# Kernel tuning notes

Measured on AMD Instinct MI355X. Metric: run time of the kernel, lower is better.

Reference implementation:

```python
import jax, jax.numpy as jnp
import numpy as np

B, C_IN, N_NODES = 128, 64, 1024
N_TRIPLES = 3 * (N_NODES - 1)  # node 0 is the shared zero vector


def _btc(x, idx, w, b):
    # x: [B, C, N]; idx: [B, 3M]; w: [O, C, 3]; b: [O]
    Bv, C, _ = x.shape
    T = idx.shape[1]
    g = jnp.take_along_axis(x, jnp.broadcast_to(idx[:, None, :], (Bv, C, T)), axis=2)
    g = g.reshape(Bv, C, T // 3, 3)  # stride-3 kernel-3 conv == per-triple contraction
    out = jnp.einsum('bcnk,ock->bon', g, w) + b[None, :, None]
    zero = jnp.zeros((Bv, out.shape[1], 1), dtype=out.dtype)
    return jnp.concatenate([zero, out], axis=2)  # re-prepend zero node -> [B, O, N]


def _tln(x):
    mean = jnp.mean(x, axis=(1, 2), keepdims=True)
    std = jnp.std(x, axis=(1, 2), ddof=1, keepdims=True)  # torch.std is unbiased
    return (x - mean) / (std + 1e-5)


def _tower(x, idx, p):
    x = jax.nn.leaky_relu(_tln(_btc(x, idx, p['w_conv1'], p['b_conv1'])), 0.01)
    x = jax.nn.leaky_relu(_tln(_btc(x, idx, p['w_conv2'], p['b_conv2'])), 0.01)
    x = _tln(_btc(x, idx, p['w_conv3'], p['b_conv3']))
    x = jnp.max(x, axis=2)  # DynamicPooling -> [B, 64]
    x = jax.nn.leaky_relu(x @ p['w_fc1'].T + p['b_fc1'], 0.01)
    return x @ p['w_fc2'].T + p['b_fc2']  # [B, 1]  (Dropout is identity at eval)


def setup_inputs() -> dict:
    key = jax.random.key(0)
    ks = jax.random.split(key, 12)
    s = 0.05
    return {
        'data1': jax.random.normal(ks[0], (B, C_IN, N_NODES), jnp.float32),
        'idx1': jax.random.randint(ks[1], (B, N_TRIPLES, 1), 0, N_NODES, dtype=jnp.int64)
                if jax.config.jax_enable_x64 else
                jax.random.randint(ks[1], (B, N_TRIPLES, 1), 0, N_NODES).astype(jnp.int32),
        'data2': jax.random.normal(ks[2], (B, C_IN, N_NODES), jnp.float32),
        'idx2': jax.random.randint(ks[3], (B, N_TRIPLES, 1), 0, N_NODES).astype(jnp.int32),
        'w_conv1': jax.random.normal(ks[4], (256, C_IN, 3), jnp.float32) * s,
        'b_conv1': jnp.zeros((256,), jnp.float32),
        'w_conv2': jax.random.normal(ks[5], (128, 256, 3), jnp.float32) * s,
        'b_conv2': jnp.zeros((128,), jnp.float32),
        'w_conv3': jax.random.normal(ks[6], (64, 128, 3), jnp.float32) * s,
        'b_conv3': jnp.zeros((64,), jnp.float32),
        'w_fc1': jax.random.normal(ks[7], (32, 64), jnp.float32) * s,
        'b_fc1': jnp.zeros((32,), jnp.float32),
        'w_fc2': jax.random.normal(ks[8], (1, 32), jnp.float32) * s,
        'b_fc2': jnp.zeros((1,), jnp.float32),
    }


def reference(data1, idx1, data2, idx2,
              w_conv1, b_conv1, w_conv2, b_conv2, w_conv3, b_conv3,
              w_fc1, b_fc1, w_fc2, b_fc2):
    p = dict(w_conv1=w_conv1, b_conv1=b_conv1, w_conv2=w_conv2, b_conv2=b_conv2,
             w_conv3=w_conv3, b_conv3=b_conv3, w_fc1=w_fc1, b_fc1=b_fc1,
             w_fc2=w_fc2, b_fc2=b_fc2)
    y1 = _tower(data1, idx1[..., 0], p)
    y2 = _tower(data2, idx2[..., 0], p)
    return jnp.squeeze(jax.nn.sigmoid(y1 - y2), axis=1)  # [B]
```

## Files before the change

### kernel.cpp

```cpp
#include <hip/hip_runtime.h>
#include <math.h>

typedef __attribute__((ext_vector_type(4))) float f32x4;
typedef __attribute__((ext_vector_type(2))) float f32x2;

#define LRELU(x) ((x) > 0.0f ? (x) : 0.01f * (x))

struct __align__(4) Int3 { int x, y, z; };

__device__ __forceinline__ float2 stats_from(const float* sums, int b, float count) {
    float s = sums[2 * b], q = sums[2 * b + 1];
    float mean = s / count;
    float var = (q - s * s / count) / (count - 1.0f);
    var = fmaxf(var, 0.0f);
    return make_float2(mean, 1.0f / (sqrtf(var) + 1e-5f));
}
__device__ __forceinline__ void atomicMaxF(float* a, float v) {
    if (v >= 0.0f) atomicMax((int*)a, __float_as_int(v));
    else           atomicMin((unsigned int*)a, __float_as_uint(v));
}
__device__ __forceinline__ unsigned int fp8x4_nact(unsigned int u, float a, float c) {
    f32x2 lo = __builtin_amdgcn_cvt_pk_f32_fp8(u, false);
    f32x2 hi = __builtin_amdgcn_cvt_pk_f32_fp8(u, true);
    lo = lo * a + c; hi = hi * a + c;
// ... 150 lines not shown
    for (int i = 0; i < 4; i++)
#pragma unroll
        for (int t = 0; t < 4; t++) acc[i][t] = (f32x4){0.f, 0.f, 0.f, 0.f};

    const unsigned char* xb = xT8 + (((size_t)b) << 10) * 64;
    const int* idxb = (b >= 128 ? idxB : idxA) + (size_t)(b & 127) * 3069;

    const int gr = tid >> 1, gh = tid & 1;
    int s0, s1, s2;
    {
        int n = nt0 + gr;
        int t0 = (n == 0) ? 0 : (n - 1);
        const Int3 sv = *(const Int3*)&idxb[3 * t0];
        s0 = sv.x; s1 = sv.y; s2 = sv.z;
    }
    const unsigned char* wrow = wq8 + (size_t)(o0 + gr) * 192;
    const int swz = gr & 7;

    uint4 g0A, g1A, g2A, g3A, w0A, w1A, w2A, w3A;
    uint4 g0B, g1B, g2B, g3B, w0B, w1B, w2B, w3B;

    {
        const int srcA = gh ? s1 : s0;
        const uint4* gp = (const uint4*)(xb + (size_t)srcA * 64);
        g0A = gp[0]; g1A = gp[1]; g2A = gp[2]; g3A = gp[3];
        const uint4* wp = (const uint4*)(wrow + (gh << 6));
        w0A = wp[0]; w1A = wp[1]; w2A = wp[2]; w3A = wp[3];
    }
    if (gh == 0) {
        const uint4* gp = (const uint4*)(xb + (size_t)s2 * 64);
        g0B = gp[0]; g1B = gp[1]; g2B = gp[2]; g3B = gp[3];
        const uint4* wp = (const uint4*)(wrow + 128);
        w0B = wp[0]; w1B = wp[1]; w2B = wp[2]; w3B = wp[3];
    }

    *(uint4*)&gt8[gr * 128 + (((gh << 2) | 0) ^ swz) * 16] = g0A;
    *(uint4*)&gt8[gr * 128 + (((gh << 2) | 1) ^ swz) * 16] = g1A;
    *(uint4*)&gt8[gr * 128 + (((gh << 2) | 2) ^ swz) * 16] = g2A;
    *(uint4*)&gt8[gr * 128 + (((gh << 2) | 3) ^ swz) * 16] = g3A;
    *(uint4*)&wt8[gr * 128 + (((gh << 2) | 0) ^ swz) * 16] = w0A;
    *(uint4*)&wt8[gr * 128 + (((gh << 2) | 1) ^ swz) * 16] = w1A;
    *(uint4*)&wt8[gr * 128 + (((gh << 2) | 2) ^ swz) * 16] = w2A;
    *(uint4*)&wt8[gr * 128 + (((gh << 2) | 3) ^ swz) * 16] = w3A;

#define MFMA_PP(PP) {                                                            \
        ulonglong2 a0v, a1v, a2v, a3v, b0v, b1v, b2v, b3v;                       \
        {                                                                        \
            const int cx = ((((PP) * 4 + quad) ^ blkid) << 4);                   \
            a0v = *(const ulonglong2*)&wt8[(wo * 64 +  0 + l15) * 128 + cx];     \
            a1v = *(const ulonglong2*)&wt8[(wo * 64 + 16 + l15) * 128 + cx];     \
            a2v = *(const ulonglong2*)&wt8[(wo * 64 + 32 + l15) * 128 + cx];     \
            a3v = *(const ulonglong2*)&wt8[(wo * 64 + 48 + l15) * 128 + cx];     \
            b0v = *(const ulonglong2*)&gt8[(wn * 64 +  0 + l15) * 128 + cx];     \
            b1v = *(const ulonglong2*)&gt8[(wn * 64 + 16 + l15) * 128 + cx];     \
            b2v = *(const ulonglong2*)&gt8[(wn * 64 + 32 + l15) * 128 + cx];     \
            b3v = *(const ulonglong2*)&gt8[(wn * 64 + 48 + l15) * 128 + cx];     \
        }                                                                        \
        acc[0][0] = __builtin_amdgcn_mfma_f32_16x16x32_fp8_fp8((long)a0v.x, (long)b0v.x, acc[0][0], 0, 0, 0); \
        acc[0][1] = __builtin_amdgcn_mfma_f32_16x16x32_fp8_fp8((long)a0v.x, (long)b1v.x, acc[0][1], 0, 0, 0); \
        acc[0][2] = __builtin_amdgcn_mfma_f32_16x16x32_fp8_fp8((long)a0v.x, (long)b2v.x, acc[0][2], 0, 0, 0); \
        acc[0][3] = __builtin_amdgcn_mfma_f32_16x16x32_fp8_fp8((long)a0v.x, (long)b3v.x, acc[0][3], 0, 0, 0); \
        acc[1][0] = __builtin_amdgcn_mfma_f32_16x16x32_fp8_fp8((long)a1v.x, (long)b0v.x, acc[1][0], 0, 0, 0); \
        acc[1][1] = __builtin_amdgcn_mfma_f32_16x16x32_fp8_fp8((long)a1v.x, (long)b1v.x, acc[1][1], 0, 0, 0); \
        acc[1][2] = __builtin_amdgcn_mfma_f32_16x16x32_fp8_fp8((long)a1v.x, (long)b2v.x, acc[1][2], 0, 0, 0); \
        acc[1][3] = __builtin_amdgcn_mfma_f32_16x16x32_fp8_fp8((long)a1v.x, (long)b3v.x, acc[1][3], 0, 0, 0); \
        acc[2][0] = __builtin_amdgcn_mfma_f32_16x16x32_fp8_fp8((long)a2v.x, (long)b0v.x, acc[2][0], 0, 0, 0); \
        acc[2][1] = __builtin_amdgcn_mfma_f32_16x16x32_fp8_fp8((long)a2v.x, (long)b1v.x, acc[2][1], 0, 0, 0); \
        acc[2][2] = __builtin_amdgcn_mfma_f32_16x16x32_fp8_fp8((long)a2v.x, (long)b2v.x, acc[2][2], 0, 0, 0); \
        acc[2][3] = __builtin_amdgcn_mfma_f32_16x16x32_fp8_fp8((long)a2v.x, (long)b3v.x, acc[2][3], 0, 0, 0); \
        acc[3][0] = __builtin_amdgcn_mfma_f32_16x16x32_fp8_fp8((long)a3v.x, (long)b0v.x, acc[3][0], 0, 0, 0); \
        acc[3][1] = __builtin_amdgcn_mfma_f32_16x16x32_fp8_fp8((long)a3v.x, (long)b1v.x, acc[3][1], 0, 0, 0); \
        acc[3][2] = __builtin_amdgcn_mfma_f32_16x16x32_fp8_fp8((long)a3v.x, (long)b2v.x, acc[3][2], 0, 0, 0); \
        acc[3][3] = __builtin_amdgcn_mfma_f32_16x16x32_fp8_fp8((long)a3v.x, (long)b3v.x, acc[3][3], 0, 0, 0); \
        acc[0][0] = __builtin_amdgcn_mfma_f32_16x16x32_fp8_fp8((long)a0v.y, (long)b0v.y, acc[0][0], 0, 0, 0); \
        acc[0][1] = __builtin_amdgcn_mfma_f32_16x16x32_fp8_fp8((long)a0v.y, (long)b1v.y, acc[0][1], 0, 0, 0); \
        acc[0][2] = __builtin_amdgcn_mfma_f32_16x16x32_fp8_fp8((long)a0v.y, (long)b2v.y, acc[0][2], 0, 0, 0); \
        acc[0][3] = __builtin_amdgcn_mfma_f32_16x16x32_fp8_fp8((long)a0v.y, (long)b3v.y, acc[0][3], 0, 0, 0); \
        acc[1][0] = __builtin_amdgcn_mfma_f32_16x16x32_fp8_fp8((long)a1v.y, (long)b0v.y, acc[1][0], 0, 0, 0); \
        acc[1][1] = __builtin_amdgcn_mfma_f32_16x16x32_fp8_fp8((long)a1v.y, (long)b1v.y, acc[1][1], 0, 0, 0); \
        acc[1][2] = __builtin_amdgcn_mfma_f32_16x16x32_fp8_fp8((long)a1v.y, (long)b2v.y, acc[1][2], 0, 0, 0); \
        acc[1][3] = __builtin_amdgcn_mfma_f32_16x16x32_fp8_fp8((long)a1v.y, (long)b3v.y, acc[1][3], 0, 0, 0); \
        acc[2][0] = __builtin_amdgcn_mfma_f32_16x16x32_fp8_fp8((long)a2v.y, (long)b0v.y, acc[2][0], 0, 0, 0); \
        acc[2][1] = __builtin_amdgcn_mfma_f32_16x16x32_fp8_fp8((long)a2v.y, (long)b1v.y, acc[2][1], 0, 0, 0); \
        acc[2][2] = __builtin_amdgcn_mfma_f32_16x16x32_fp8_fp8((long)a2v.y, (long)b2v.y, acc[2][2], 0, 0, 0); \
        acc[2][3] = __builtin_amdgcn_mfma_f32_16x16x32_fp8_fp8((long)a2v.y, (long)b3v.y, acc[2][3], 0, 0, 0); \
        acc[3][0] = __builtin_amdgcn_mfma_f32_16x16x32_fp8_fp8((long)a3v.y, (long)b0v.y, acc[3][0], 0, 0, 0); \
        acc[3][1] = __builtin_amdgcn_mfma_f32_16x16x32_fp8_fp8((long)a3v.y, (long)b1v.y, acc[3][1], 0, 0, 0); \
        acc[3][2] = __builtin_amdgcn_mfma_f32_16x16x32_fp8_fp8((long)a3v.y, (long)b2v.y, acc[3][2], 0, 0, 0); \
        acc[3][3] = __builtin_amdgcn_mfma_f32_16x16x32_fp8_fp8((long)a3v.y, (long)b3v.y, acc[3][3], 0, 0, 0); \
    }

    __syncthreads();
    MFMA_PP(0);
    MFMA_PP(1);
    __syncthreads();
    if (gh == 0) {
        *(uint4*)&gt8[gr * 128 + ((0 ^ swz) * 16)] = g0B;
        *(uint4*)&gt8[gr * 128 + ((1 ^ swz) * 16)] = g1B;
        *(uint4*)&gt8[gr * 128 + ((2 ^ swz) * 16)] = g2B;
        *(uint4*)&gt8[gr * 128 + ((3 ^ swz) * 16)] = g3B;
        *(uint4*)&wt8[gr * 128 + ((0 ^ swz) * 16)] = w0B;
        *(uint4*)&wt8[gr * 128 + ((1 ^ swz) * 16)] = w1B;
        *(uint4*)&wt8[gr * 128 + ((2 ^ swz) * 16)] = w2B;
        *(uint4*)&wt8[gr * 128 + ((3 ^ swz) * 16)] = w3B;
    }
    __syncthreads();
    MFMA_PP(0);
#undef MFMA_PP

    __syncthreads();
    unsigned char* eb = gt8;
    float lsum = 0.f, lsq = 0.f;
#pragma unroll
    for (int i = 0; i < 4; i++) {
        const int obl = wo * 64 + i * 16 + quad * 4;
        const int op  = perm128(obl);
        const float4 bv = *(const float4*)(bias + o0 + obl);
#pragma unroll
        for (int t = 0; t < 4; t++) {
            const int nl = wn * 64 + t * 16 + l15;
            float v0 = acc[i][t][0] + bv.x;
            float v1 = acc[i][t][1] + bv.y;
            float v2 = acc[i][t][2] + bv.z;
            float v3 = acc[i][t][3] + bv.w;
            if (nt0 + nl == 0) { v0 = v1 = v2 = v3 = 0.f; }
            lsum += v0 + v1 + v2 + v3;
            lsq  += v0 * v0 + v1 * v1 + v2 * v2 + v3 * v3;
            int r = __builtin_amdgcn_cvt_pk_fp8_f32(v0, v1, 0, false);
            r = __builtin_amdgcn_cvt_pk_fp8_f32(v2, v3, r, true);
            *(unsigned int*)&eb[nl * 128 + (op ^ ((nl & 7) << 4))] = (unsigned int)r;
        }
    }
#pragma unroll
    for (int off = 32; off > 0; off >>= 1) {
        lsum += __shfl_down(lsum, off);
        lsq  += __shfl_down(lsq, off);
    }
    float* red = (float*)wt8;
    if (lane == 0) { red[wave] = lsum; red[4 + wave] = lsq; }
    __syncthreads();
#pragma unroll
    for (int c = 0; c < 4; ++c) {
        const int ch = c * 256 + tid;
        const int row = ch >> 3, off = (ch & 7) << 4;
        uint4 v = *(const uint4*)&eb[row * 128 + (off ^ ((row & 7) << 4))];
        *(uint4*)&out[((size_t)b * 1024 + nt0 + row) * 256 + o0 + off] = v;
    }
    if (tid == 0) {
        atomicAdd(&sums[2 * b + 0], red[0] + red[1] + red[2] + red[3]);
        atomicAdd(&sums[2 * b + 1], red[4] + red[5] + red[6] + red[7]);
    }
}

__global__ __launch_bounds__(256, 3) void conv2_fp8(
    const unsigned char* __restrict__ a1,
    const int* __restrict__ idxA,
    const int* __restrict__ idxB,
    const unsigned char* __restrict__ wq8,
    const float* __restrict__ bias,
    unsigned char* __restrict__ out,
    float* __restrict__ sums)
{
    const int b   = blockIdx.x;
    const int nt0 = blockIdx.z << 7;
    const int tid = threadIdx.x;
    const int lane = tid & 63, wave = tid >> 6;
    const int wo = wave & 1, wn = wave >> 1;
    const int quad = lane >> 4, l15 = lane & 15;
    const int blkid = lane & 7;

    __shared__ __align__(16) unsigned char wt8[128 * 128];
    __shared__ __align__(16) unsigned char gt8[128 * 128];

    f32x4 acc[4][4];
#pragma unroll
    for (int i = 0; i < 4; i++)
#pragma unroll
        for (int t = 0; t < 4; t++) acc[i][t] = (f32x4){0.f, 0.f, 0.f, 0.f};

    const unsigned char* xb = a1 + (((size_t)b) << 10) * 256;
    const int* idxb = (b >= 128 ? idxB : idxA) + (size_t)(b & 127) * 3069;

    const int gr = tid >> 1, gh = tid & 1;
    int si0, si1, si2;
    {
        int n = nt0 + gr;
        int t0 = (n == 0) ? 0 : (n - 1);
        const Int3 sv = *(const Int3*)&idxb[3 * t0];
        si0 = sv.x; si1 = sv.y; si2 = sv.z;
    }
    const unsigned char* wrow = wq8 + (size_t)gr * 768 + gh * 64;
    const int swz = gr & 7;

    uint4 g0A, g1A, g2A, g3A;
    uint4 g0B, g1B, g2B, g3B;

#define LOADC2(S, KC) {                                                          \
        const int j_  = (KC) >> 1;                                               \
        const int c0_ = ((KC) & 1) << 7;                                         \
        const int src_ = (j_ == 0) ? si0 : ((j_ == 1) ? si1 : si2);              \
        const uint4* gp_ = (const uint4*)(xb + (size_t)src_ * 256 + c0_ + gh * 64); \
        g0##S = gp_[0]; g1##S = gp_[1]; g2##S = gp_[2]; g3##S = gp_[3];          \
    }

#define STAGE2(S, KC) {                                                          \
        const uint4* wp_ = (const uint4*)(wrow + (KC) * 128);                    \
        uint4 wv0 = wp_[0], wv1 = wp_[1], wv2 = wp_[2], wv3 = wp_[3];            \
        *(uint4*)&gt8[gr * 128 + (((gh << 2) | 0) ^ swz) * 16] = g0##S;          \
        *(uint4*)&gt8[gr * 128 + (((gh << 2) | 1) ^ swz) * 16] = g1##S;          \
        *(uint4*)&gt8[gr * 128 + (((gh << 2) | 2) ^ swz) * 16] = g2##S;          \
        *(uint4*)&gt8[gr * 128 + (((gh << 2) | 3) ^ swz) * 16] = g3##S;          \
        *(uint4*)&wt8[gr * 128 + (((gh << 2) | 0) ^ swz) * 16] = wv0;            \
        *(uint4*)&wt8[gr * 128 + (((gh << 2) | 1) ^ swz) * 16] = wv1;            \
        *(uint4*)&wt8[gr * 128 + (((gh << 2) | 2) ^ swz) * 16] = wv2;            \
        *(uint4*)&wt8[gr * 128 + (((gh << 2) | 3) ^ swz) * 16] = wv3;            \
    }

#define MFMA_STEP2 {                                                             \
        _Pragma("unroll")                                                        \
        for (int pp = 0; pp < 2; ++pp) {                                         \
            ulonglong2 a0v, a1v, a2v, a3v, b0v, b1v, b2v, b3v;                   \
            {                                                                    \
                const int cx = (((pp * 4 + quad) ^ blkid) << 4);                 \
                a0v = *(const ulonglong2*)&wt8[(wo * 64 +  0 + l15) * 128 + cx]; \
                a1v = *(const ulonglong2*)&wt8[(wo * 64 + 16 + l15) * 128 + cx]; \
                a2v = *(const ulonglong2*)&wt8[(wo * 64 + 32 + l15) * 128 + cx]; \
                a3v = *(const ulonglong2*)&wt8[(wo * 64 + 48 + l15) * 128 + cx]; \
                b0v = *(const ulonglong2*)&gt8[(wn * 64 +  0 + l15) * 128 + cx]; \
                b1v = *(const ulonglong2*)&gt8[(wn * 64 + 16 + l15) * 128 + cx]; \
                b2v = *(const ulonglong2*)&gt8[(wn * 64 + 32 + l15) * 128 + cx]; \
                b3v = *(const ulonglong2*)&gt8[(wn * 64 + 48 + l15) * 128 + cx]; \
            }                                                                    \
            acc[0][0] = __builtin_amdgcn_mfma_f32_16x16x32_fp8_fp8((long)a0v.x, (long)b0v.x, acc[0][0], 0, 0, 0); \
            acc[0][1] = __builtin_amdgcn_mfma_f32_16x16x32_fp8_fp8((long)a0v.x, (long)b1v.x, acc[0][1], 0, 0, 0); \
            acc[0][2] = __builtin_amdgcn_mfma_f32_16x16x32_fp8_fp8((long)a0v.x, (long)b2v.x, acc[0][2], 0, 0, 0); \
            acc[0][3] = __builtin_amdgcn_mfma_f32_16x16x32_fp8_fp8((long)a0v.x, (long)b3v.x, acc[0][3], 0, 0, 0); \
            acc[1][0] = __builtin_amdgcn_mfma_f32_16x16x32_fp8_fp8((long)a1v.x, (long)b0v.x, acc[1][0], 0, 0, 0); \
            acc[1][1] = __builtin_amdgcn_mfma_f32_16x16x32_fp8_fp8((long)a1v.x, (long)b1v.x, acc[1][1], 0, 0, 0); \
            acc[1][2] = __builtin_amdgcn_mfma_f32_16x16x32_fp8_fp8((long)a1v.x, (long)b2v.x, acc[1][2], 0, 0, 0); \
            acc[1][3] = __builtin_amdgcn_mfma_f32_16x16x32_fp8_fp8((long)a1v.x, (long)b3v.x, acc[1][3], 0, 0, 0); \
            acc[2][0] = __builtin_amdgcn_mfma_f32_16x16x32_fp8_fp8((long)a2v.x, (long)b0v.x, acc[2][0], 0, 0, 0); \
            acc[2][1] = __builtin_amdgcn_mfma_f32_16x16x32_fp8_fp8((long)a2v.x, (long)b1v.x, acc[2][1], 0, 0, 0); \
            acc[2][2] = __builtin_amdgcn_mfma_f32_16x16x32_fp8_fp8((long)a2v.x, (long)b2v.x, acc[2][2], 0, 0, 0); \
            acc[2][3] = __builtin_amdgcn_mfma_f32_16x16x32_fp8_fp8((long)a2v.x, (long)b3v.x, acc[2][3], 0, 0, 0); \
            acc[3][0] = __builtin_amdgcn_mfma_f32_16x16x32_fp8_fp8((long)a3v.x, (long)b0v.x, acc[3][0], 0, 0, 0); \
            acc[3][1] = __builtin_amdgcn_mfma_f32_16x16x32_fp8_fp8((long)a3v.x, (long)b1v.x, acc[3][1], 0, 0, 0); \
            acc[3][2] = __builtin_amdgcn_mfma_f32_16x16x32_fp8_fp8((long)a3v.x, (long)b2v.x, acc[3][2], 0, 0, 0); \
            acc[3][3] = __builtin_amdgcn_mfma_f32_16x16x32_fp8_fp8((long)a3v.x, (long)b3v.x, acc[3][3], 0, 0, 0); \
            acc[0][0] = __builtin_amdgcn_mfma_f32_16x16x32_fp8_fp8((long)a0v.y, (long)b0v.y, acc[0][0], 0, 0, 0); \
            acc[0][1] = __builtin_amdgcn_mfma_f32_16x16x32_fp8_fp8((long)a0v.y, (long)b1v.y, acc[0][1], 0, 0, 0); \
            acc[0][2] = __builtin_amdgcn_mfma_f32_16x16x32_fp8_fp8((long)a0v.y, (long)b2v.y, acc[0][2], 0, 0, 0); \
            acc[0][3] = __builtin_amdgcn_mfma_f32_16x16x32_fp8_fp8((long)a0v.y, (long)b3v.y, acc[0][3], 0, 0, 0); \
            acc[1][0] = __builtin_amdgcn_mfma_f32_16x16x32_fp8_fp8((long)a1v.y, (long)b0v.y, acc[1][0], 0, 0, 0); \
            acc[1][1] = __builtin_amdgcn_mfma_f32_16x16x32_fp8_fp8((long)a1v.y, (long)b1v.y, acc[1][1], 0, 0, 0); \
            acc[1][2] = __builtin_amdgcn_mfma_f32_16x16x32_fp8_fp8((long)a1v.y, (long)b2v.y, acc[1][2], 0, 0, 0); \
            acc[1][3] = __builtin_amdgcn_mfma_f32_16x16x32_fp8_fp8((long)a1v.y, (long)b3v.y, acc[1][3], 0, 0, 0); \
            acc[2][0] = __builtin_amdgcn_mfma_f32_16x16x32_fp8_fp8((long)a2v.y, (long)b0v.y, acc[2][0], 0, 0, 0); \
            acc[2][1] = __builtin_amdgcn_mfma_f32_16x16x32_fp8_fp8((long)a2v.y, (long)b1v.y, acc[2][1], 0, 0, 0); \
            acc[2][2] = __builtin_amdgcn_mfma_f32_16x16x32_fp8_fp8((long)a2v.y, (long)b2v.y, acc[2][2], 0, 0, 0); \
            acc[2][3] = __builtin_amdgcn_mfma_f32_16x16x32_fp8_fp8((long)a2v.y, (long)b3v.y, acc[2][3], 0, 0, 0); \
            acc[3][0] = __builtin_amdgcn_mfma_f32_16x16x32_fp8_fp8((long)a3v.y, (long)b0v.y, acc[3][0], 0, 0, 0); \
            acc[3][1] = __builtin_amdgcn_mfma_f32_16x16x32_fp8_fp8((long)a3v.y, (long)b1v.y, acc[3][1], 0, 0, 0); \
            acc[3][2] = __builtin_amdgcn_mfma_f32_16x16x32_fp8_fp8((long)a3v.y, (long)b2v.y, acc[3][2], 0, 0, 0); \
            acc[3][3] = __builtin_amdgcn_mfma_f32_16x16x32_fp8_fp8((long)a3v.y, (long)b3v.y, acc[3][3], 0, 0, 0); \
        }                                                                        \
    }

    LOADC2(A, 0);
    LOADC2(B, 1);
    int kc = 0;
    for (; kc + 2 <= 6; kc += 2) {
        if (kc) __syncthreads();
        STAGE2(A, kc);
        if (kc + 2 < 6) LOADC2(A, kc + 2);
        __syncthreads();
        MFMA_STEP2;
        __syncthreads();
        STAGE2(B, kc + 1);
        if (kc + 3 < 6) LOADC2(B, kc + 3);
        __syncthreads();
        MFMA_STEP2;
    }
#undef LOADC2
#undef STAGE2
#undef MFMA_STEP2

    __syncthreads();
    unsigned char* eb = gt8;
    float lsum = 0.f, lsq = 0.f;
#pragma unroll
    for (int i = 0; i < 4; i++) {
        const int obl = wo * 64 + i * 16 + quad * 4;
        const int op  = perm128(obl);
        const float4 bv = *(const float4*)(bias + obl);
#pragma unroll
        for (int t = 0; t < 4; t++) {
            const int nl = wn * 64 + t * 16 + l15;
            float v0 = acc[i][t][0] + bv.x;
            float v1 = acc[i][t][1] + bv.y;
            float v2 = acc[i][t][2] + bv.z;
            float v3 = acc[i][t][3] + bv.w;
            if (nt0 + nl == 0) { v0 = v1 = v2 = v3 = 0.f; }
            lsum += v0 + v1 + v2 + v3;
            lsq  += v0 * v0 + v1 * v1 + v2 * v2 + v3 * v3;
            int r = __builtin_amdgcn_cvt_pk_fp8_f32(v0, v1, 0, false);
            r = __builtin_amdgcn_cvt_pk_fp8_f32(v2, v3, r, true);
            *(unsigned int*)&eb[nl * 128 + (op ^ ((nl & 7) << 4))] = (unsigned int)r;
        }
    }
#pragma unroll
    for (int off = 32; off > 0; off >>= 1) {
        lsum += __shfl_down(lsum, off);
        lsq  += __shfl_down(lsq, off);
    }
    float* red = (float*)wt8;
    if (lane == 0) { red[wave] = lsum; red[4 + wave] = lsq; }
    __syncthreads();
#pragma unroll
    for (int c = 0; c < 4; ++c) {
        const int ch = c * 256 + tid;
        const int row = ch >> 3, off = (ch & 7) << 4;
        uint4 v = *(const uint4*)&eb[row * 128 + (off ^ ((row & 7) << 4))];
        *(uint4*)&out[((size_t)b * 1024 + nt0 + row) * 128 + off] = v;
    }
    if (tid == 0) {
        atomicAdd(&sums[2 * b + 0], red[0] + red[1] + red[2] + red[3]);
        atomicAdd(&sums[2 * b + 1], red[4] + red[5] + red[6] + red[7]);
    }
}

__global__ __launch_bounds__(256, 3) void conv3_fp8(
    const unsigned char* __restrict__ a2,
    const int* __restrict__ idxA,
    const int* __restrict__ idxB,
    const unsigned char* __restrict__ wq8,
    const float* __restrict__ bias,
    float* __restrict__ sums,
    float* __restrict__ pmax)
{
    const int b   = blockIdx.x;
    const int nt0 = blockIdx.z << 7;
    const int tid = threadIdx.x;
    const int lane = tid & 63, wave = tid >> 6;
    const int wo = wave & 1, wn = wave >> 1;
    const int quad = lane >> 4, l15 = lane & 15;
    const int blkid = lane & 7;

    __shared__ __align__(16) unsigned char wt8[64 * 128];
    __shared__ __align__(16) unsigned char gt8[128 * 128];

    f32x4 acc[2][4];
#pragma unroll
    for (int i = 0; i < 2; i++)
#pragma unroll
        for (int t = 0; t < 4; t++) acc[i][t] = (f32x4){0.f, 0.f, 0.f, 0.f};

    const unsigned char* xb = a2 + (((size_t)b) << 10) * 128;
    const int* idxb = (b >= 128 ? idxB : idxA) + (size_t)(b & 127) * 3069;

    const int gr = tid >> 1, gh = tid & 1;
    int si0, si1, si2;
    {
        int n = nt0 + gr;
        int t0 = (n == 0) ? 0 : (n - 1);
        const Int3 sv = *(const Int3*)&idxb[3 * t0];
        si0 = sv.x; si1 = sv.y; si2 = sv.z;
    }
    const int wr = tid >> 2, wseg = tid & 3;
    const unsigned char* wrow = wq8 + (size_t)wr * 384 + wseg * 32;
    const int gswz = gr & 7, wswz = wr & 7;

    uint4 g0A, g1A, g2A, g3A;
    uint4 g0B, g1B, g2B, g3B;

#define LOADC3(S, KC) {                                                          \
        const int src_ = ((KC) == 0) ? si0 : (((KC) == 1) ? si1 : si2);          \
        const uint4* gp_ = (const uint4*)(xb + (size_t)src_ * 128 + gh * 64);    \
        g0##S = gp_[0]; g1##S = gp_[1]; g2##S = gp_[2]; g3##S = gp_[3];          \
    }

#define STAGE3(S, KC) {                                                          \
        const uint4* wp_ = (const uint4*)(wrow + (KC) * 128);                    \
        uint4 wv0 = wp_[0], wv1 = wp_[1];                                        \
        *(uint4*)&gt8[gr * 128 + (((gh << 2) | 0) ^ gswz) * 16] = g0##S;         \
        *(uint4*)&gt8[gr * 128 + (((gh << 2) | 1) ^ gswz) * 16] = g1##S;         \
        *(uint4*)&gt8[gr * 128 + (((gh << 2) | 2) ^ gswz) * 16] = g2##S;         \
        *(uint4*)&gt8[gr * 128 + (((gh << 2) | 3) ^ gswz) * 16] = g3##S;         \
        *(uint4*)&wt8[wr * 128 + (((wseg << 1) | 0) ^ wswz) * 16] = wv0;         \
        *(uint4*)&wt8[wr * 128 + (((wseg << 1) | 1) ^ wswz) * 16] = wv1;         \
    }

#define MFMA_STEP3 {                                                             \
        _Pragma("unroll")                                                        \
        for (int pp = 0; pp < 2; ++pp) {                                         \
            ulonglong2 a0v, a1v, b0v, b1v, b2v, b3v;                             \
            {                                                                    \
                const int cx = (((pp * 4 + quad) ^ blkid) << 4);                 \
                a0v = *(const ulonglong2*)&wt8[(wo * 32 +  0 + l15) * 128 + cx]; \
                a1v = *(const ulonglong2*)&wt8[(wo * 32 + 16 + l15) * 128 + cx]; \
                b0v = *(const ulonglong2*)&gt8[(wn * 64 +  0 + l15) * 128 + cx]; \
                b1v = *(const ulonglong2*)&gt8[(wn * 64 + 16 + l15) * 128 + cx]; \
                b2v = *(const ulonglong2*)&gt8[(wn * 64 + 32 + l15) * 128 + cx]; \
                b3v = *(const ulonglong2*)&gt8[(wn * 64 + 48 + l15) * 128 + cx]; \
            }                                                                    \
            acc[0][0] = __builtin_amdgcn_mfma_f32_16x16x32_fp8_fp8((long)a0v.x, (long)b0v.x, acc[0][0], 0, 0, 0); \
            acc[0][1] = __builtin_amdgcn_mfma_f32_16x16x32_fp8_fp8((long)a0v.x, (long)b1v.x, acc[0][1], 0, 0, 0); \
            acc[0][2] = __builtin_amdgcn_mfma_f32_16x16x32_fp8_fp8((long)a0v.x, (long)b2v.x, acc[0][2], 0, 0, 0); \
            acc[0][3] = __builtin_amdgcn_mfma_f32_16x16x32_fp8_fp8((long)a0v.x, (long)b3v.x, acc[0][3], 0, 0, 0); \
            acc[1][0] = __builtin_amdgcn_mfma_f32_16x16x32_fp8_fp8((long)a1v.x, (long)b0v.x, acc[1][0], 0, 0, 0); \
            acc[1][1] = __builtin_amdgcn_mfma_f32_16x16x32_fp8_fp8((long)a1v.x, (long)b1v.x, acc[1][1], 0, 0, 0); \
            acc[1][2] = __builtin_amdgcn_mfma_f32_16x16x32_fp8_fp8((long)a1v.x, (long)b2v.x, acc[1][2], 0, 0, 0); \
            acc[1][3] = __builtin_amdgcn_mfma_f32_16x16x32_fp8_fp8((long)a1v.x, (long)b3v.x, acc[1][3], 0, 0, 0); \
            acc[0][0] = __builtin_amdgcn_mfma_f32_16x16x32_fp8_fp8((long)a0v.y, (long)b0v.y, acc[0][0], 0, 0, 0); \
            acc[0][1] = __builtin_amdgcn_mfma_f32_16x16x32_fp8_fp8((long)a0v.y, (long)b1v.y, acc[0][1], 0, 0, 0); \
            acc[0][2] = __builtin_amdgcn_mfma_f32_16x16x32_fp8_fp8((long)a0v.y, (long)b2v.y, acc[0][2], 0, 0, 0); \
            acc[0][3] = __builtin_amdgcn_mfma_f32_16x16x32_fp8_fp8((long)a0v.y, (long)b3v.y, acc[0][3], 0, 0, 0); \
            acc[1][0] = __builtin_amdgcn_mfma_f32_16x16x32_fp8_fp8((long)a1v.y, (long)b0v.y, acc[1][0], 0, 0, 0); \
            acc[1][1] = __builtin_amdgcn_mfma_f32_16x16x32_fp8_fp8((long)a1v.y, (long)b1v.y, acc[1][1], 0, 0, 0); \
            acc[1][2] = __builtin_amdgcn_mfma_f32_16x16x32_fp8_fp8((long)a1v.y, (long)b2v.y, acc[1][2], 0, 0, 0); \
            acc[1][3] = __builtin_amdgcn_mfma_f32_16x16x32_fp8_fp8((long)a1v.y, (long)b3v.y, acc[1][3], 0, 0, 0); \
        }                                                                        \
    }

    LOADC3(A, 0);
    LOADC3(B, 1);
    int kc = 0;
    for (; kc + 2 <= 3; kc += 2) {
        if (kc) __syncthreads();
        STAGE3(A, kc);
        if (kc + 2 < 3) LOADC3(A, kc + 2);
        __syncthreads();
        MFMA_STEP3;
        __syncthreads();
        STAGE3(B, kc + 1);
        __syncthreads();
        MFMA_STEP3;
    }
    {
        __syncthreads();
        STAGE3(A, 2);
        __syncthreads();
        MFMA_STEP3;
    }
#undef LOADC3
#undef STAGE3
#undef MFMA_STEP3

    __syncthreads();
    float lsum = 0.f, lsq = 0.f;
#pragma unroll
    for (int i = 0; i < 2; i++) {
        const int ob = wo * 32 + i * 16 + quad * 4;
        const float4 bv = *(const float4*)(bias + ob);
        float mx0 = -1e30f, mx1 = -1e30f, mx2 = -1e30f, mx3 = -1e30f;
#pragma unroll
        for (int t = 0; t < 4; t++) {
            const int n = nt0 + wn * 64 + t * 16 + l15;
            float v0 = acc[i][t][0] + bv.x;
            float v1 = acc[i][t][1] + bv.y;
            float v2 = acc[i][t][2] + bv.z;
            float v3 = acc[i][t][3] + bv.w;
            if (n == 0) { v0 = v1 = v2 = v3 = 0.f; }
            lsum += v0 + v1 + v2 + v3;
            lsq  += v0 * v0 + v1 * v1 + v2 * v2 + v3 * v3;
            mx0 = fmaxf(mx0, v0); mx1 = fmaxf(mx1, v1);
            mx2 = fmaxf(mx2, v2); mx3 = fmaxf(mx3, v3);
        }
#pragma unroll
        for (int off = 1; off < 16; off <<= 1) {
            mx0 = fmaxf(mx0, __shfl_xor(mx0, off));
            mx1 = fmaxf(mx1, __shfl_xor(mx1, off));
            mx2 = fmaxf(mx2, __shfl_xor(mx2, off));
            mx3 = fmaxf(mx3, __shfl_xor(mx3, off));
        }
        if (l15 == 0) {
            atomicMaxF(&pmax[(size_t)b * 64 + ob + 0], mx0);
            atomicMaxF(&pmax[(size_t)b * 64 + ob + 1], mx1);
            atomicMaxF(&pmax[(size_t)b * 64 + ob + 2], mx2);
            atomicMaxF(&pmax[(size_t)b * 64 + ob + 3], mx3);
        }
    }
#pragma unroll
    for (int off = 32; off > 0; off >>= 1) {
        lsum += __shfl_down(lsum, off);
        lsq  += __shfl_down(lsq, off);
    }
    float* red = (float*)wt8;
    if (lane == 0) { red[wave] = lsum; red[4 + wave] = lsq; }
    __syncthreads();
    if (tid == 0) {
        atomicAdd(&sums[2 * b + 0], red[0] + red[1] + red[2] + red[3]);
        atomicAdd(&sums[2 * b + 1], red[4] + red[5] + red[6] + red[7]);
    }
}

__global__ __launch_bounds__(64) void fc_head(
    const float* __restrict__ pmax, const float* __restrict__ sums3, float count,
    const float* __restrict__ w_fc1, const float* __restrict__ b_fc1,
    const float* __restrict__ w_fc2, const float* __restrict__ b_fc2,
    float* __restrict__ y)
{
    const int b = blockIdx.x, t = threadIdx.x;
    __shared__ float pooled[64];
    __shared__ float hid[32];
    float2 s = stats_from(sums3, b, count);
    pooled[t] = (pmax[(size_t)b * 64 + t] - s.x) * s.y;
    __syncthreads();
    if (t < 32) {
        float h = b_fc1[t];
#pragma unroll
        for (int c = 0; c < 64; c++) h += pooled[c] * w_fc1[t * 64 + c];
        hid[t] = LRELU(h);
    }
    __syncthreads();
    if (t == 0) {
        float v = b_fc2[0];
#pragma unroll
        for (int c = 0; c < 32; c++) v += hid[c] * w_fc2[c];
        y[b] = v;
    }
}

__global__ void sigmoid_diff(const float* __restrict__ y1,
                             const float* __restrict__ y2,
                             float* __restrict__ out)
{
    int b = threadIdx.x;
    if (b < 128) out[b] = 1.0f / (1.0f + expf(-(y1[b] - y2[b])));
}

extern "C" void kernel_launch(void* const* d_in, const int* in_sizes, int n_in,
                              void* d_out, int out_size, void* d_ws, size_t ws_size,
                              hipStream_t stream)
{
    const float* data1 = (const float*)d_in[0];
    const int*   idx1  = (const int*)d_in[1];
    const float* data2 = (const float*)d_in[2];
    const int*   idx2  = (const int*)d_in[3];
    const float* w1 = (const float*)d_in[4];
    const float* b1 = (const float*)d_in[5];
    const float* w2 = (const float*)d_in[6];
    const float* b2 = (const float*)d_in[7];
    const float* w3 = (const float*)d_in[8];
    const float* b3 = (const float*)d_in[9];
    const float* wfc1 = (const float*)d_in[10];
    const float* bfc1 = (const float*)d_in[11];
    const float* wfc2 = (const float*)d_in[12];
    const float* bfc2 = (const float*)d_in[13];

    const size_t needM = (size_t)256 * 1024 * (64 + 256 + 128) + 768 * 1024;
    const bool merged = ws_size >= needM;
    const int nB = merged ? 256 : 128;
    const size_t szXT = (size_t)nB * 1024 * 64;
    const size_t szA1 = (size_t)nB * 1024 * 256;
    const size_t szA2 = (size_t)nB * 1024 * 128;

    char* ws = (char*)d_ws;
    unsigned char* xT8 = (unsigned char*)ws;
    unsigned char* a1  = (unsigned char*)(ws + szXT);
    unsigned char* a2  = (unsigned char*)(ws + szXT + szA1);
    char* tail = ws + szXT + szA1 + szA2;
    unsigned char* wq1f8 = (unsigned char*)tail;
    unsigned char* wq2f8 = (unsigned char*)(tail + 128 * 1024);
    unsigned char* wq3f8 = (unsigned char*)(tail + 384 * 1024);
    float* sums = (float*)(tail + 448 * 1024);
    float* pmax = (float*)(tail + 512 * 1024);
    float* yv   = (float*)(tail + 640 * 1024);

    prep_all<<<96, 256, 0, stream>>>(w1, wq1f8, w2, wq2f8, w3, wq3f8);

    const int nIter = merged ? 1 : 2;
    for (int t = 0; t < nIter; ++t) {
        const float* dA = (merged || t == 0) ? data1 : data2;
        const float* dB = merged ? data2 : dA;
        const int* iA = (merged || t == 0) ? idx1 : idx2;
        const int* iB = merged ? idx2 : iA;
        float* s1 = sums;
        float* s2 = sums + nB * 2;
        float* s3 = sums + nB * 4;

        transpose_in<<<dim3(16, nB), 256, 0, stream>>>(dA, dB, xT8, sums,
                                                       (unsigned int*)pmax);

        conv1_fp8<<<dim3(nB, 2, 8), 256, 0, stream>>>(
            xT8, iA, iB, wq1f8, b1, a1, s1);

        norm_act_fp8<<<dim3(16, nB), 256, 0, stream>>>(a1, s1, 256.0f * 1024.0f, 16384);

        conv2_fp8<<<dim3(nB, 1, 8), 256, 0, stream>>>(
            a1, iA, iB, wq2f8, b2, a2, s2);

        norm_act_fp8<<<dim3(8, nB), 256, 0, stream>>>(a2, s2, 128.0f * 1024.0f, 8192);

        conv3_fp8<<<dim3(nB, 1, 8), 256, 0, stream>>>(
            a2, iA, iB, wq3f8, b3, s3, pmax);

        fc_head<<<nB, 64, 0, stream>>>(pmax, s3, 64.0f * 1024.0f,
                                       wfc1, bfc1, wfc2, bfc2,
                                       yv + (merged ? 0 : t * 128));
    }
    sigmoid_diff<<<1, 128, 0, stream>>>(yv, yv + 128, (float*)d_out);
}
```

Baseline: 263.9 us.

## Make conv2/conv3 blocks persistent over four node tiles with register-resident weights

conv2 and conv3 now launch a quarter as many blocks along z, and each block loops over four 128-node tiles. The fp8 weight slices are loaded into registers once per block and reused across all four tiles instead of being reloaded from global memory for every tile. Per-block sum/sumsq reductions and their atomics are amortised over four tiles. The trade-off is more registers (conv2 launch bounds drop from 3 to 2 blocks per CU), fewer blocks to spread across CUs, and serialized tiles within a block with extra barriers.

```diff
diff --git a/kernel.cpp b/kernel.cpp
--- a/kernel.cpp
+++ b/kernel.cpp
@@ -326,7 +326,7 @@
     }
 }
 
-__global__ __launch_bounds__(256, 3) void conv2_fp8(
+__global__ __launch_bounds__(256, 2) void conv2_fp8(
     const unsigned char* __restrict__ a1,
     const int* __restrict__ idxA,
     const int* __restrict__ idxB,
@@ -335,8 +335,8 @@
     unsigned char* __restrict__ out,
     float* __restrict__ sums)
 {
-    const int b   = blockIdx.x;
-    const int nt0 = blockIdx.z << 7;
+    const int b  = blockIdx.x;
+    const int zg = blockIdx.z;
     const int tid = threadIdx.x;
     const int lane = tid & 63, wave = tid >> 6;
     const int wo = wave & 1, wn = wave >> 1;
@@ -346,25 +346,20 @@
     __shared__ __align__(16) unsigned char wt8[128 * 128];
     __shared__ __align__(16) unsigned char gt8[128 * 128];
 
-    f32x4 acc[4][4];
-#pragma unroll
-    for (int i = 0; i < 4; i++)
-#pragma unroll
-        for (int t = 0; t < 4; t++) acc[i][t] = (f32x4){0.f, 0.f, 0.f, 0.f};
-
     const unsigned char* xb = a1 + (((size_t)b) << 10) * 256;
     const int* idxb = (b >= 128 ? idxB : idxA) + (size_t)(b & 127) * 3069;
 
     const int gr = tid >> 1, gh = tid & 1;
-    int si0, si1, si2;
-    {
-        int n = nt0 + gr;
-        int t0 = (n == 0) ? 0 : (n - 1);
-        const Int3 sv = *(const Int3*)&idxb[3 * t0];
-        si0 = sv.x; si1 = sv.y; si2 = sv.z;
-    }
     const unsigned char* wrow = wq8 + (size_t)gr * 768 + gh * 64;
     const int swz = gr & 7;
+
+    uint4 wv00, wv01, wv02, wv03, wv10, wv11, wv12, wv13,
+          wv20, wv21, wv22, wv23, wv30, wv31, wv32, wv33,
+          wv40, wv41, wv42, wv43, wv50, wv51, wv52, wv53;
+#define LDW(C) { const uint4* wp_ = (const uint4*)(wrow + (C) * 128);            \
+        wv##C##0 = wp_[0]; wv##C##1 = wp_[1]; wv##C##2 = wp_[2]; wv##C##3 = wp_[3]; }
+    LDW(0) LDW(1) LDW(2) LDW(3) LDW(4) LDW(5)
+#undef LDW
 
     uint4 g0A, g1A, g2A, g3A;
     uint4 g0B, g1B, g2B, g3B;
@@ -378,16 +373,14 @@
     }
 
 #define STAGE2(S, KC) {                                                          \
-        const uint4* wp_ = (const uint4*)(wrow + (KC) * 128);                    \
-        uint4 wv0 = wp_[0], wv1 = wp_[1], wv2 = wp_[2], wv3 = wp_[3];            \
         *(uint4*)&gt8[gr * 128 + (((gh << 2) | 0) ^ swz) * 16] = g0##S;          \
         *(uint4*)&gt8[gr * 128 + (((gh << 2) | 1) ^ swz) * 16] = g1##S;          \
         *(uint4*)&gt8[gr * 128 + (((gh << 2) | 2) ^ swz) * 16] = g2##S;          \
         *(uint4*)&gt8[gr * 128 + (((gh << 2) | 3) ^ swz) * 16] = g3##S;          \
-        *(uint4*)&wt8[gr * 128 + (((gh << 2) | 0) ^ swz) * 16] = wv0;            \
-        *(uint4*)&wt8[gr * 128 + (((gh << 2) | 1) ^ swz) * 16] = wv1;            \
-        *(uint4*)&wt8[gr * 128 + (((gh << 2) | 2) ^ swz) * 16] = wv2;            \
-        *(uint4*)&wt8[gr * 128 + (((gh << 2) | 3) ^ swz) * 16] = wv3;            \
+        *(uint4*)&wt8[gr * 128 + (((gh << 2) | 0) ^ swz) * 16] = wv##KC##0;      \
+        *(uint4*)&wt8[gr * 128 + (((gh << 2) | 1) ^ swz) * 16] = wv##KC##1;      \
+        *(uint4*)&wt8[gr * 128 + (((gh << 2) | 2) ^ swz) * 16] = wv##KC##2;      \
+        *(uint4*)&wt8[gr * 128 + (((gh << 2) | 3) ^ swz) * 16] = wv##KC##3;      \
     }
 
 #define MFMA_STEP2 {                                                             \
@@ -440,48 +433,76 @@
         }                                                                        \
     }
 
-    LOADC2(A, 0);
-    LOADC2(B, 1);
-    int kc = 0;
-    for (; kc + 2 <= 6; kc += 2) {
-        if (kc) __syncthreads();
-        STAGE2(A, kc);
-        if (kc + 2 < 6) LOADC2(A, kc + 2);
+    float lsum = 0.f, lsq = 0.f;
+
+    for (int s = 0; s < 4; ++s) {
+        const int nt0 = ((zg << 2) | s) << 7;
+
+        f32x4 acc[4][4];
+#pragma unroll
+        for (int i = 0; i < 4; i++)
+#pragma unroll
+            for (int t = 0; t < 4; t++) acc[i][t] = (f32x4){0.f, 0.f, 0.f, 0.f};
+
+        int si0, si1, si2;
+        {
+            int n = nt0 + gr;
+            int t0 = (n == 0) ? 0 : (n - 1);
+            const Int3 sv = *(const Int3*)&idxb[3 * t0];
+            si0 = sv.x; si1 = sv.y; si2 = sv.z;
+        }
+
+        LOADC2(A, 0);
+        LOADC2(B, 1);
+        STAGE2(A, 0); LOADC2(A, 2);
+        __syncthreads(); MFMA_STEP2; __syncthreads();
+        STAGE2(B, 1); LOADC2(B, 3);
+        __syncthreads(); MFMA_STEP2; __syncthreads();
+        STAGE2(A, 2); LOADC2(A, 4);
+        __syncthreads(); MFMA_STEP2; __syncthreads();
+        STAGE2(B, 3); LOADC2(B, 5);
+        __syncthreads(); MFMA_STEP2; __syncthreads();
+        STAGE2(A, 4);
+        __syncthreads(); MFMA_STEP2; __syncthreads();
+        STAGE2(B, 5);
+        __syncthreads(); MFMA_STEP2;
+
         __syncthreads();
-        MFMA_STEP2;
+        unsigned char* eb = gt8;
+#pragma unroll
+        for (int i = 0; i < 4; i++) {
+            const int obl = wo * 64 + i * 16 + quad * 4;
+            const int op  = perm128(obl);
+            const float4 bv = *(const float4*)(bias + obl);
+#pragma unroll
+            for (int t = 0; t < 4; t++) {
+                const int nl = wn * 64 + t * 16 + l15;
+                float v0 = acc[i][t][0] + bv.x;
+                float v1 = acc[i][t][1] + bv.y;
+                float v2 = acc[i][t][2] + bv.z;
+                float v3 = acc[i][t][3] + bv.w;
+                if (nt0 + nl == 0) { v0 = v1 = v2 = v3 = 0.f; }
+                lsum += v0 + v1 + v2 + v3;
+                lsq  += v0 * v0 + v1 * v1 + v2 * v2 + v3 * v3;
+                int r = __builtin_amdgcn_cvt_pk_fp8_f32(v0, v1, 0, false);
+                r = __builtin_amdgcn_cvt_pk_fp8_f32(v2, v3, r, true);
+                *(unsigned int*)&eb[nl * 128 + (op ^ ((nl & 7) << 4))] = (unsigned int)r;
+            }
+        }
         __syncthreads();
-        STAGE2(B, kc + 1);
-        if (kc + 3 < 6) LOADC2(B, kc + 3);
+#pragma unroll
+        for (int c = 0; c < 4; ++c) {
+            const int ch = c * 256 + tid;
+            const int row = ch >> 3, off = (ch & 7) << 4;
+            uint4 v = *(const uint4*)&eb[row * 128 + (off ^ ((row & 7) << 4))];
+            *(uint4*)&out[((size_t)b * 1024 + nt0 + row) * 128 + off] = v;
+        }
         __syncthreads();
-        MFMA_STEP2;
     }
 #undef LOADC2
 #undef STAGE2
 #undef MFMA_STEP2
 
-    __syncthreads();
-    unsigned char* eb = gt8;
-    float lsum = 0.f, lsq = 0.f;
-#pragma unroll
-    for (int i = 0; i < 4; i++) {
-        const int obl = wo * 64 + i * 16 + quad * 4;
-        const int op  = perm128(obl);
-        const float4 bv = *(const float4*)(bias + obl);
-#pragma unroll
-        for (int t = 0; t < 4; t++) {
-            const int nl = wn * 64 + t * 16 + l15;
-            float v0 = acc[i][t][0] + bv.x;
-            float v1 = acc[i][t][1] + bv.y;
-            float v2 = acc[i][t][2] + bv.z;
-            float v3 = acc[i][t][3] + bv.w;
-            if (nt0 + nl == 0) { v0 = v1 = v2 = v3 = 0.f; }
-            lsum += v0 + v1 + v2 + v3;
-            lsq  += v0 * v0 + v1 * v1 + v2 * v2 + v3 * v3;
-            int r = __builtin_amdgcn_cvt_pk_fp8_f32(v0, v1, 0, false);
-            r = __builtin_amdgcn_cvt_pk_fp8_f32(v2, v3, r, true);
-            *(unsigned int*)&eb[nl * 128 + (op ^ ((nl & 7) << 4))] = (unsigned int)r;
-        }
-    }
 #pragma unroll
     for (int off = 32; off > 0; off >>= 1) {
         lsum += __shfl_down(lsum, off);
@@ -490,13 +511,6 @@
     float* red = (float*)wt8;
     if (lane == 0) { red[wave] = lsum; red[4 + wave] = lsq; }
     __syncthreads();
-#pragma unroll
-    for (int c = 0; c < 4; ++c) {
-        const int ch = c * 256 + tid;
-        const int row = ch >> 3, off = (ch & 7) << 4;
-        uint4 v = *(const uint4*)&eb[row * 128 + (off ^ ((row & 7) << 4))];
-        *(uint4*)&out[((size_t)b * 1024 + nt0 + row) * 128 + off] = v;
-    }
     if (tid == 0) {
         atomicAdd(&sums[2 * b + 0], red[0] + red[1] + red[2] + red[3]);
         atomicAdd(&sums[2 * b + 1], red[4] + red[5] + red[6] + red[7]);
@@ -512,8 +526,8 @@
     float* __restrict__ sums,
     float* __restrict__ pmax)
 {
-    const int b   = blockIdx.x;
-    const int nt0 = blockIdx.z << 7;
+    const int b  = blockIdx.x;
+    const int zg = blockIdx.z;
     const int tid = threadIdx.x;
     const int lane = tid & 63, wave = tid >> 6;
     const int wo = wave & 1, wn = wave >> 1;
@@ -523,26 +537,19 @@
     __shared__ __align__(16) unsigned char wt8[64 * 128];
     __shared__ __align__(16) unsigned char gt8[128 * 128];
 
-    f32x4 acc[2][4];
-#pragma unroll
-    for (int i = 0; i < 2; i++)
-#pragma unroll
-        for (int t = 0; t < 4; t++) acc[i][t] = (f32x4){0.f, 0.f, 0.f, 0.f};
-
     const unsigned char* xb = a2 + (((size_t)b) << 10) * 128;
     const int* idxb = (b >= 128 ? idxB : idxA) + (size_t)(b & 127) * 3069;
 
     const int gr = tid >> 1, gh = tid & 1;
-    int si0, si1, si2;
-    {
-        int n = nt0 + gr;
-        int t0 = (n == 0) ? 0 : (n - 1);
-        const Int3 sv = *(const Int3*)&idxb[3 * t0];
-        si0 = sv.x; si1 = sv.y; si2 = sv.z;
-    }
     const int wr = tid >> 2, wseg = tid & 3;
     const unsigned char* wrow = wq8 + (size_t)wr * 384 + wseg * 32;
     const int gswz = gr & 7, wswz = wr & 7;
+
+    uint4 wv00, wv01, wv10, wv11, wv20, wv21;
+#define LDW3(C) { const uint4* wp_ = (const uint4*)(wrow + (C) * 128);           \
+        wv##C##0 = wp_[0]; wv##C##1 = wp_[1]; }
+    LDW3(0) LDW3(1) LDW3(2)
+#undef LDW3
 
     uint4 g0A, g1A, g2A, g3A;
     uint4 g0B, g1B, g2B, g3B;
@@ -554,14 +561,12 @@
     }
 
 #define STAGE3(S, KC) {                                                          \
-        const uint4* wp_ = (const uint4*)(wrow + (KC) * 128);                    \
-        uint4 wv0 = wp_[0], wv1 = wp_[1];                                        \
         *(uint4*)&gt8[gr * 128 + (((gh << 2) | 0) ^ gswz) * 16] = g0##S;         \
         *(uint4*)&gt8[gr * 128 + (((gh << 2) | 1) ^ gswz) * 16] = g1##S;         \
         *(uint4*)&gt8[gr * 128 + (((gh << 2) | 2) ^ gswz) * 16] = g2##S;         \
         *(uint4*)&gt8[gr * 128 + (((gh << 2) | 3) ^ gswz) * 16] = g3##S;         \
-        *(uint4*)&wt8[wr * 128 + (((wseg << 1) | 0) ^ wswz) * 16] = wv0;         \
-        *(uint4*)&wt8[wr * 128 + (((wseg << 1) | 1) ^ wswz) * 16] = wv1;         \
+        *(uint4*)&wt8[wr * 128 + (((wseg << 1) | 0) ^ wswz) * 16] = wv##KC##0;   \
+        *(uint4*)&wt8[wr * 128 + (((wseg << 1) | 1) ^ wswz) * 16] = wv##KC##1;   \
     }
 
 #define MFMA_STEP3 {                                                             \
@@ -596,69 +601,78 @@
         }                                                                        \
     }
 
-    LOADC3(A, 0);
-    LOADC3(B, 1);
-    int kc = 0;
-    for (; kc + 2 <= 3; kc += 2) {
-        if (kc) __syncthreads();
-        STAGE3(A, kc);
-        if (kc + 2 < 3) LOADC3(A, kc + 2);
-        __syncthreads();
-        MFMA_STEP3;
-        __syncthreads();
-        STAGE3(B, kc + 1);
-        __syncthreads();
-        MFMA_STEP3;
-    }
-    {
-        __syncthreads();
+    float lsum = 0.f, lsq = 0.f;
+
+    for (int s = 0; s < 4; ++s) {
+        const int nt0 = ((zg << 2) | s) << 7;
+
+        f32x4 acc[2][4];
+#pragma unroll
+        for (int i = 0; i < 2; i++)
+#pragma unroll
+            for (int t = 0; t < 4; t++) acc[i][t] = (f32x4){0.f, 0.f, 0.f, 0.f};
+
+        int si0, si1, si2;
+        {
+            int n = nt0 + gr;
+            int t0 = (n == 0) ? 0 : (n - 1);
+            const Int3 sv = *(const Int3*)&idxb[3 * t0];
+            si0 = sv.x; si1 = sv.y; si2 = sv.z;
+        }
+
+        if (s) __syncthreads();
+        LOADC3(A, 0);
+        LOADC3(B, 1);
+        STAGE3(A, 0); LOADC3(A, 2);
+        __syncthreads(); MFMA_STEP3; __syncthreads();
+        STAGE3(B, 1);
+        __syncthreads(); MFMA_STEP3; __syncthreads();
         STAGE3(A, 2);
-        __syncthreads();
-        MFMA_STEP3;
+        __syncthreads(); MFMA_STEP3;
+
+#pragma unroll
+        for (int i = 0; i < 2; i++) {
+            const int ob = wo * 32 + i * 16 + quad * 4;
+            const float4 bv = *(const float4*)(bias + ob);
+            float mx0 = -1e30f, mx1 = -1e30f, mx2 = -1e30f, mx3 = -1e30f;
+#pragma unroll
+            for (int t = 0; t < 4; t++) {
+                const int n = nt0 + wn * 64 + t * 16 + l15;
+                float v0 = acc[i][t][0] + bv.x;
+                float v1 = acc[i][t][1] + bv.y;
+                float v2 = acc[i][t][2] + bv.z;
+                float v3 = acc[i][t][3] + bv.w;
+                if (n == 0) { v0 = v1 = v2 = v3 = 0.f; }
+                lsum += v0 + v1 + v2 + v3;
+                lsq  += v0 * v0 + v1 * v1 + v2 * v2 + v3 * v3;
+                mx0 = fmaxf(mx0, v0); mx1 = fmaxf(mx1, v1);
+                mx2 = fmaxf(mx2, v2); mx3 = fmaxf(mx3, v3);
+            }
+#pragma unroll
+            for (int off = 1; off < 16; off <<= 1) {
+                mx0 = fmaxf(mx0, __shfl_xor(mx0, off));
+                mx1 = fmaxf(mx1, __shfl_xor(mx1, off));
+                mx2 = fmaxf(mx2, __shfl_xor(mx2, off));
+                mx3 = fmaxf(mx3, __shfl_xor(mx3, off));
+            }
+            if (l15 == 0) {
+                atomicMaxF(&pmax[(size_t)b * 64 + ob + 0], mx0);
+                atomicMaxF(&pmax[(size_t)b * 64 + ob + 1], mx1);
+                atomicMaxF(&pmax[(size_t)b * 64 + ob + 2], mx2);
+                atomicMaxF(&pmax[(size_t)b * 64 + ob + 3], mx3);
+            }
+        }
     }
 #undef LOADC3
 #undef STAGE3
 #undef MFMA_STEP3
 
-    __syncthreads();
-    float lsum = 0.f, lsq = 0.f;
-#pragma unroll
-    for (int i = 0; i < 2; i++) {
-        const int ob = wo * 32 + i * 16 + quad * 4;
-        const float4 bv = *(const float4*)(bias + ob);
-        float mx0 = -1e30f, mx1 = -1e30f, mx2 = -1e30f, mx3 = -1e30f;
-#pragma unroll
-        for (int t = 0; t < 4; t++) {
-            const int n = nt0 + wn * 64 + t * 16 + l15;
-            float v0 = acc[i][t][0] + bv.x;
-            float v1 = acc[i][t][1] + bv.y;
-            float v2 = acc[i][t][2] + bv.z;
-            float v3 = acc[i][t][3] + bv.w;
-            if (n == 0) { v0 = v1 = v2 = v3 = 0.f; }
-            lsum += v0 + v1 + v2 + v3;
-            lsq  += v0 * v0 + v1 * v1 + v2 * v2 + v3 * v3;
-            mx0 = fmaxf(mx0, v0); mx1 = fmaxf(mx1, v1);
-            mx2 = fmaxf(mx2, v2); mx3 = fmaxf(mx3, v3);
-        }
-#pragma unroll
-        for (int off = 1; off < 16; off <<= 1) {
-            mx0 = fmaxf(mx0, __shfl_xor(mx0, off));
-            mx1 = fmaxf(mx1, __shfl_xor(mx1, off));
-            mx2 = fmaxf(mx2, __shfl_xor(mx2, off));
-            mx3 = fmaxf(mx3, __shfl_xor(mx3, off));
-        }
-        if (l15 == 0) {
-            atomicMaxF(&pmax[(size_t)b * 64 + ob + 0], mx0);
-            atomicMaxF(&pmax[(size_t)b * 64 + ob + 1], mx1);
-            atomicMaxF(&pmax[(size_t)b * 64 + ob + 2], mx2);
-            atomicMaxF(&pmax[(size_t)b * 64 + ob + 3], mx3);
-        }
-    }
 #pragma unroll
     for (int off = 32; off > 0; off >>= 1) {
         lsum += __shfl_down(lsum, off);
         lsq  += __shfl_down(lsq, off);
     }
+    __syncthreads();
     float* red = (float*)wt8;
     if (lane == 0) { red[wave] = lsum; red[4 + wave] = lsq; }
     __syncthreads();
@@ -761,12 +775,12 @@
 
         norm_act_fp8<<<dim3(16, nB), 256, 0, stream>>>(a1, s1, 256.0f * 1024.0f, 16384);
 
-        conv2_fp8<<<dim3(nB, 1, 8), 256, 0, stream>>>(
+        conv2_fp8<<<dim3(nB, 1, 2), 256, 0, stream>>>(
             a1, iA, iB, wq2f8, b2, a2, s2);
 
         norm_act_fp8<<<dim3(8, nB), 256, 0, stream>>>(a2, s2, 128.0f * 1024.0f, 8192);
 
-        conv3_fp8<<<dim3(nB, 1, 8), 256, 0, stream>>>(
+        conv3_fp8<<<dim3(nB, 1, 2), 256, 0, stream>>>(
             a2, iA, iB, wq3f8, b3, s3, pmax);
 
         fc_head<<<nB, 64, 0, stream>>>(pmax, s3, 64.0f * 1024.0f,
```

New measurement: 317.6 us. +20.4%, slower.
